# Optimization experiments

Hardware: AMD Instinct MI355X
Metric: run time of the kernel (lower is better)

The kernel has to match this reference:

```python
import jax, jax.numpy as jnp
import numpy as np

TEMPERATURE = 1.0

def setup_inputs() -> dict:
    key = jax.random.key(0)
    k1, k2 = jax.random.split(key)
    B, I, O = 256, 1024, 1024
    x = jax.random.normal(k1, (B, I), dtype=jnp.float32)
    # mimic TruncatedNormal(stddev=1/sqrt(input_size)) init
    w = jax.random.normal(k2, (I, O), dtype=jnp.float32) * (1.0 / np.sqrt(I))
    b = jnp.zeros((O,), dtype=jnp.float32)
    return {"x": x, "w": w, "b": b}

def reference(x, w, b):
    # z: [B, I, O] outer product per sample
    z = jnp.einsum('bi,io->bio', x, w)
    n = x.shape[-1]
    # per-output-neuron temperature softmax over the input dim I
    s = jax.nn.softmax(jnp.abs(z) / TEMPERATURE, axis=1)
    out = n * jnp.sum(z * s, axis=1)  # [B, O]
    return out + b
```

## Files before the change

kernel.cpp:

```cpp
#include <hip/hip_runtime.h>

#define BDIM 256
#define IDIM 1024
#define ODIM 1024

#define TILE_O 64
#define TILE_B 4
#define CH 64

typedef float v2f __attribute__((ext_vector_type(2)));

#if __has_builtin(__builtin_amdgcn_exp2f)
#define FAST_EXP2(v) __builtin_amdgcn_exp2f(v)
#else
#define FAST_EXP2(v) exp2f(v)
#endif

__global__ __launch_bounds__(256, 8)
void softmax_t_linear_kernel(const float* __restrict__ x,
                             const float* __restrict__ w,
                             const float* __restrict__ bias,
                             float* __restrict__ out) {
  __shared__ float ws[CH][TILE_O];
  __shared__ float xs[TILE_B][CH];

  const int tx = threadIdx.x;
  const int ty = threadIdx.y;
  const int tid = ty * 64 + tx;
  const int o0 = blockIdx.x * TILE_O;
  const int b0 = blockIdx.y * TILE_B;

  const float LOG2E = 1.4426950408889634f;
  const float* xrow = x + (size_t)(b0 + ty) * IDIM;

  v2f num = {0.0f, 0.0f};
  v2f den = {0.0f, 0.0f};

  for (int i0 = 0; i0 < IDIM; i0 += CH) {
    __syncthreads();
    if (tx < CH / 4) {
      float4 v = *(const float4*)(xrow + i0 + tx * 4);
      v.x *= LOG2E; v.y *= LOG2E; v.z *= LOG2E; v.w *= LOG2E;
      *(float4*)(&xs[ty][tx * 4]) = v;
    }
#pragma unroll
    for (int k = 0; k < 4; ++k) {
      int f = tid + k * 256;
      int row = f >> 4;
      int col = f & 15;
      *(float4*)(&ws[row][col * 4]) =
          *(const float4*)(w + (size_t)(i0 + row) * ODIM + o0 + col * 4);
    }
    __syncthreads();

#pragma unroll 4
    for (int j = 0; j < CH; j += 8) {
      float4 xq0 = *(const float4*)(&xs[ty][j]);
      float4 xq1 = *(const float4*)(&xs[ty][j + 4]);
      float wv[8];
#pragma unroll
      for (int u = 0; u < 8; ++u) wv[u] = ws[j + u][tx];
      v2f p0 = {xq0.x * wv[0], xq0.y * wv[1]};
      v2f p1 = {xq0.z * wv[2], xq0.w * wv[3]};
      v2f p2 = {xq1.x * wv[4], xq1.y * wv[5]};
      v2f p3 = {xq1.z * wv[6], xq1.w * wv[7]};
      v2f t0, t1, t2, t3;
      t0.x = FAST_EXP2(__builtin_fabsf(p0.x));
      t0.y = FAST_EXP2(__builtin_fabsf(p0.y));
      t1.x = FAST_EXP2(__builtin_fabsf(p1.x));
      t1.y = FAST_EXP2(__builtin_fabsf(p1.y));
      t2.x = FAST_EXP2(__builtin_fabsf(p2.x));
      t2.y = FAST_EXP2(__builtin_fabsf(p2.y));
      t3.x = FAST_EXP2(__builtin_fabsf(p3.x));
      t3.y = FAST_EXP2(__builtin_fabsf(p3.y));
      num += p0 * t0; den += t0;
      num += p1 * t1; den += t1;
      num += p2 * t2; den += t2;
      num += p3 * t3; den += t3;
    }
  }

  const float LN2 = 0.6931471805599453f;
  const float scale = (float)IDIM * LN2;
  const float numv = num.x + num.y;
  const float denv = den.x + den.y;
  const int o = o0 + tx;
  out[(size_t)(b0 + ty) * ODIM + o] = scale * numv / denv + bias[o];
}

extern "C" void kernel_launch(void* const* d_in, const int* in_sizes, int n_in,
                              void* d_out, int out_size, void* d_ws, size_t ws_size,
                              hipStream_t stream) {
  const float* x = (const float*)d_in[0];
  const float* w = (const float*)d_in[1];
  const float* b = (const float*)d_in[2];
  float* out = (float*)d_out;

  dim3 grid(ODIM / TILE_O, BDIM / TILE_B);
  dim3 block(64, 4);
  softmax_t_linear_kernel<<<grid, block, 0, stream>>>(x, w, b, out);
}
```

Baseline: 103.1 us.

## Split input dimension across blocks with partial sums and register prefetch

Splits the softmax reduction over the input dimension into two halves handled by separate blocks. Each block writes partial numerator and denominator sums to workspace, and a second kernel combines them and applies scale and bias. It also prefetches the next weight and x chunk into registers while the current chunk is processed. This is meant to raise occupancy and overlap global loads with compute, at the cost of an extra launch and partial-sum memory traffic.

```diff
diff --git a/kernel.cpp b/kernel.cpp
--- a/kernel.cpp
+++ b/kernel.cpp
@@ -7,6 +7,9 @@
 #define TILE_O 64
 #define TILE_B 4
 #define CH 64
+#define ISPLIT 2
+#define IHALF (IDIM / ISPLIT)
+#define NCH (IHALF / CH)
 
 typedef float v2f __attribute__((ext_vector_type(2)));
 
@@ -17,10 +20,9 @@
 #endif
 
 __global__ __launch_bounds__(256, 8)
-void softmax_t_linear_kernel(const float* __restrict__ x,
-                             const float* __restrict__ w,
-                             const float* __restrict__ bias,
-                             float* __restrict__ out) {
+void stl_partial_kernel(const float* __restrict__ x,
+                        const float* __restrict__ w,
+                        float2* __restrict__ part) {
   __shared__ float ws[CH][TILE_O];
   __shared__ float xs[TILE_B][CH];
 
@@ -29,27 +31,42 @@
   const int tid = ty * 64 + tx;
   const int o0 = blockIdx.x * TILE_O;
   const int b0 = blockIdx.y * TILE_B;
+  const int half = blockIdx.z;
+  const int ibase = half * IHALF;
 
   const float LOG2E = 1.4426950408889634f;
-  const float* xrow = x + (size_t)(b0 + ty) * IDIM;
+  const float* xrow = x + (size_t)(b0 + ty) * IDIM + ibase;
+
+  const int wrow[4] = {(tid) >> 4, (tid + 256) >> 4, (tid + 512) >> 4, (tid + 768) >> 4};
+  const int wcol = tid & 15;
+
+  float4 wreg[4];
+  float4 xreg;
+#pragma unroll
+  for (int k = 0; k < 4; ++k)
+    wreg[k] = *(const float4*)(w + (size_t)(ibase + wrow[k]) * ODIM + o0 + wcol * 4);
+  if (tx < CH / 4) xreg = *(const float4*)(xrow + tx * 4);
 
   v2f num = {0.0f, 0.0f};
   v2f den = {0.0f, 0.0f};
 
-  for (int i0 = 0; i0 < IDIM; i0 += CH) {
+  for (int c = 0; c < NCH; ++c) {
     __syncthreads();
     if (tx < CH / 4) {
-      float4 v = *(const float4*)(xrow + i0 + tx * 4);
+      float4 v = xreg;
       v.x *= LOG2E; v.y *= LOG2E; v.z *= LOG2E; v.w *= LOG2E;
       *(float4*)(&xs[ty][tx * 4]) = v;
     }
 #pragma unroll
-    for (int k = 0; k < 4; ++k) {
-      int f = tid + k * 256;
-      int row = f >> 4;
-      int col = f & 15;
-      *(float4*)(&ws[row][col * 4]) =
-          *(const float4*)(w + (size_t)(i0 + row) * ODIM + o0 + col * 4);
+    for (int k = 0; k < 4; ++k)
+      *(float4*)(&ws[wrow[k]][wcol * 4]) = wreg[k];
+
+    if (c + 1 < NCH) {
+      const int i1 = ibase + (c + 1) * CH;
+#pragma unroll
+      for (int k = 0; k < 4; ++k)
+        wreg[k] = *(const float4*)(w + (size_t)(i1 + wrow[k]) * ODIM + o0 + wcol * 4);
+      if (tx < CH / 4) xreg = *(const float4*)(xrow + (c + 1) * CH + tx * 4);
     }
     __syncthreads();
 
@@ -80,12 +97,22 @@
     }
   }
 
+  const int o = o0 + tx;
+  part[(size_t)half * (BDIM * ODIM) + (size_t)(b0 + ty) * ODIM + o] =
+      make_float2(num.x + num.y, den.x + den.y);
+}
+
+__global__ __launch_bounds__(256)
+void stl_combine_kernel(const float2* __restrict__ part,
+                        const float* __restrict__ bias,
+                        float* __restrict__ out) {
+  const int idx = blockIdx.x * 256 + threadIdx.x;
+  const int o = idx & (ODIM - 1);
+  const float2 a = part[idx];
+  const float2 b = part[BDIM * ODIM + idx];
   const float LN2 = 0.6931471805599453f;
   const float scale = (float)IDIM * LN2;
-  const float numv = num.x + num.y;
-  const float denv = den.x + den.y;
-  const int o = o0 + tx;
-  out[(size_t)(b0 + ty) * ODIM + o] = scale * numv / denv + bias[o];
+  out[idx] = scale * (a.x + b.x) / (a.y + b.y) + bias[o];
 }
 
 extern "C" void kernel_launch(void* const* d_in, const int* in_sizes, int n_in,
@@ -95,8 +122,11 @@
   const float* w = (const float*)d_in[1];
   const float* b = (const float*)d_in[2];
   float* out = (float*)d_out;
+  float2* part = (float2*)d_ws;
 
-  dim3 grid(ODIM / TILE_O, BDIM / TILE_B);
+  dim3 grid(ODIM / TILE_O, BDIM / TILE_B, ISPLIT);
   dim3 block(64, 4);
-  softmax_t_linear_kernel<<<grid, block, 0, stream>>>(x, w, b, out);
+  stl_partial_kernel<<<grid, block, 0, stream>>>(x, w, part);
+
+  stl_combine_kernel<<<(BDIM * ODIM) / 256, 256, 0, stream>>>(part, b, out);
 }
```

After: 139.4 us. 1.35x slower.
